# Optimization experiments

Measured on AMD Instinct MI355X. Metric: run time of the kernel, lower is better.

## Reference

```python
import jax, jax.numpy as jnp
import numpy as np

N = 50000      # nodes
E = 800000     # edges (avg degree 16)
D_IN = 128     # input_dim
H = 64         # hidden_dim (== output_dim)
L = 3          # num_layers


def setup_inputs() -> dict:
    key = jax.random.key(0)
    ks = jax.random.split(key, 24)
    s = 0.05
    p = lambda k, shape: jax.random.normal(k, shape, dtype=jnp.float32) * s
    inp = {}
    inp["node_features"] = jax.random.normal(ks[0], (N, D_IN), dtype=jnp.float32)
    inp["edge_index"] = jax.random.randint(ks[1], (2, E), 0, N, dtype=jnp.int32)
    # pre_mlp: Linear-ReLU-Linear (setup_LRL_nn with hidden_sizes=[hidden_dim])
    inp["pre_w1"] = p(ks[2], (D_IN, H)); inp["pre_b1"] = jnp.zeros((H,), jnp.float32)
    inp["pre_w2"] = p(ks[3], (H, H));    inp["pre_b2"] = jnp.zeros((H,), jnp.float32)
    # learnable skip gates (initialized to ones as in the module)
    inp["skip"] = jnp.ones((L, L), jnp.float32)
    # SAGEConv layers: lin_l (on mean-aggregated neighbors, with bias) + lin_r (root)
    for i in range(L):
        din = H * (i + 1)
        inp[f"wl{i}"] = p(ks[4 + 3 * i], (din, H))
        inp[f"bl{i}"] = jnp.zeros((H,), jnp.float32)
        inp[f"wr{i}"] = p(ks[5 + 3 * i], (din, H))
    # post_mlp: 256->64, 64->64, 64->256, 256->64
    inp["post_w1"] = p(ks[14], (H * (L + 1), H)); inp["post_b1"] = jnp.zeros((H,), jnp.float32)
    inp["post_w2"] = p(ks[15], (H, H));           inp["post_b2"] = jnp.zeros((H,), jnp.float32)
    inp["post_w3"] = p(ks[16], (H, 256));         inp["post_b3"] = jnp.zeros((256,), jnp.float32)
    inp["post_w4"] = p(ks[17], (256, H));         inp["post_b4"] = jnp.zeros((H,), jnp.float32)
    return inp


def _sage(x, src, dst, inv_deg, wl, bl, wr):
    # PyG SAGEConv (mean aggr): lin_l(mean_{j->i} x_j) + lin_r(x_i)
    agg = jax.ops.segment_sum(x[src], dst, num_segments=N) * inv_deg  # [N, Din]
    return agg @ wl + bl + x @ wr


def reference(node_features, edge_index,
              pre_w1, pre_b1, pre_w2, pre_b2, skip,
              wl0, bl0, wr0, wl1, bl1, wr1, wl2, bl2, wr2,
              post_w1, post_b1, post_w2, post_b2, post_w3, post_b3, post_w4, post_b4):
    src, dst = edge_index[0], edge_index[1]
    deg = jax.ops.segment_sum(jnp.ones((E,), jnp.float32), dst, num_segments=N)
    inv_deg = (1.0 / jnp.maximum(deg, 1.0))[:, None]  # [N,1]

    # pre_mlp
    x = jax.nn.relu(node_features @ pre_w1 + pre_b1) @ pre_w2 + pre_b2  # [N,H]

    layers = [(wl0, bl0, wr0), (wl1, bl1, wr1), (wl2, bl2, wr2)]
    all_emb = [x]
    emb = x
    for i, (wl, bl, wr) in enumerate(layers):
        gates = jax.nn.sigmoid(skip[i, :i + 1])  # [i+1]
        curr = jnp.concatenate([all_emb[j] * gates[j] for j in range(i + 1)], axis=1)  # [N, H*(i+1)]
        h = jax.nn.relu(_sage(curr, src, dst, inv_deg, wl, bl, wr))  # [N,H]  (dropout p=0)
        emb = jnp.concatenate([emb, h], axis=1)
        all_emb.append(h)

    s = jnp.sum(emb, axis=-2)  # sums over all nodes -> [H*(L+1)] (faithful to source)
    h = jax.nn.leaky_relu(s @ post_w1 + post_b1, negative_slope=0.1)
    h = jax.nn.relu(h @ post_w2 + post_b2)
    h = jax.nn.relu(h @ post_w3 + post_b3)
    return h @ post_w4 + post_b4  # [H]
```

## Files before the change

kernel.cpp:

```cpp
#include <hip/hip_runtime.h>
#include <math.h>

#define NN 50000
#define NE 800000
#define NB 196
#define SLOT 8192
#define PBH 8192

typedef float v4f __attribute__((ext_vector_type(4)));
typedef float v2f __attribute__((ext_vector_type(2)));
typedef _Float16 v8h __attribute__((ext_vector_type(8)));

__device__ __forceinline__ unsigned char enc8(float v) {
#if __has_builtin(__builtin_amdgcn_cvt_pk_fp8_f32)
  return (unsigned char)(__builtin_amdgcn_cvt_pk_fp8_f32(v, v, 0, false) & 0xFF);
#else
  unsigned u = __float_as_uint(v);
  unsigned s = (u >> 24) & 0x80u;
  unsigned au = u & 0x7fffffffu;
  float a = __uint_as_float(au);
  if (au < 0x3C800000u) {
    int m = (int)(a * 512.0f + 0.5f);
    if (m >= 8) return (unsigned char)(s | 8u);
    return (unsigned char)(s | (unsigned)m);
  }
  unsigned r = au + 0x7FFFFu + ((au >> 20) & 1u);
  unsigned e = (r >> 23) - 120u;
  unsigned man = (r >> 20) & 7u;
  if (e > 15u) { e = 15u; man = 6u; }
  return (unsigned char)(s | (e << 3) | man);
#endif
}

#if __has_builtin(__builtin_amdgcn_cvt_pk_f32_fp8)
#define DEC8_HW 1
#else
__device__ __forceinline__ float dec8_1(unsigned b) {
  unsigned s = (b & 0x80u) << 24;
  unsigned em = b & 0x7fu;
  float v;
  if (em >= 8u) v = __uint_as_float((((em >> 3) + 120u) << 23) | ((em & 7u) << 20));
  else v = (float)em * 0.001953125f;
  return __uint_as_float(__float_as_uint(v) | s);
}
#endif

__device__ __forceinline__ void dec8x8(uint2 u, float* f) {
#ifdef DEC8_HW
  v2f p0 = __builtin_amdgcn_cvt_pk_f32_fp8((int)u.x, false);
  v2f p1 = __builtin_amdgcn_cvt_pk_f32_fp8((int)u.x, true);
  v2f p2 = __builtin_amdgcn_cvt_pk_f32_fp8((int)u.y, false);
  v2f p3 = __builtin_amdgcn_cvt_pk_f32_fp8((int)u.y, true);
  f[0] = p0.x; f[1] = p0.y; f[2] = p1.x; f[3] = p1.y;
  f[4] = p2.x; f[5] = p2.y; f[6] = p3.x; f[7] = p3.y;
#else
#pragma unroll
  for (int i = 0; i < 4; ++i) f[i] = dec8_1((u.x >> (8 * i)) & 0xFF);
#pragma unroll
  for (int i = 0; i < 4; ++i) f[4 + i] = dec8_1((u.y >> (8 * i)) & 0xFF);
#endif
// ... 79 lines not shown
    if (e < NE) {
      int p = base[bk[i]] + lp[i];
      if (p < (bk[i] + 1) * SLOT) ebuf[p] = pk[i];
    }
  }
}

__global__ __launch_bounds__(256) void k_bbuild2(const unsigned* __restrict__ ebuf,
                                                 const int* __restrict__ gcur,
                                                 int* __restrict__ offs,
                                                 int* __restrict__ ends,
                                                 float* __restrict__ invd,
                                                 int* __restrict__ csr) {
  __shared__ int dcnt[256];
  __shared__ int cur[256];
  int t = threadIdx.x;
  int b = blockIdx.x;
  int node0 = b << 8;
  int es = b * SLOT;
  int ee = es + min(gcur[b], SLOT);
  dcnt[t] = 0;
  __syncthreads();
  for (int e = es + t; e < ee; e += 256) atomicAdd(&dcnt[ebuf[e] & 255], 1);
  __syncthreads();
  int v = dcnt[t];
  cur[t] = v;
  __syncthreads();
  for (int o = 1; o < 256; o <<= 1) {
    int u = (t >= o) ? cur[t - o] : 0;
    __syncthreads();
    cur[t] += u;
    __syncthreads();
  }
  int excl = cur[t] - v;
  int node = node0 + t;
  if (node < NN) {
    offs[node] = es + excl;
    ends[node] = es + excl + v;
    invd[node] = 1.0f / fmaxf((float)v, 1.0f);
  }
  __syncthreads();
  cur[t] = es + excl;
  __syncthreads();
  for (int e = es + t; e < ee; e += 256) {
    unsigned pk = ebuf[e];
    int p = atomicAdd(&cur[pk & 255], 1);
    csr[p] = (int)(pk >> 8);
  }
}

struct CArgs {
  const float* nf; const _Float16* wpk;
  const float* preb1; const float* preb2;
  const float* bl0; const float* bl1; const float* bl2;
  const int* offs; const int* ends; const int* csr; const float* invd;
  _Float16 *x, *h0, *h1, *m0, *m1;
  unsigned char *f8a, *f8b;
  float* sv;
  int* done;
  const float *pw1, *pb1, *pw2, *pb2, *pw3, *pb3, *pw4, *pb4;
  float* outp;
  int n;
};

__device__ __forceinline__ void gather_tile(int t, int n0,
    const unsigned char* __restrict__ fb, const int* __restrict__ offs,
    const int* __restrict__ ends, const int* __restrict__ csr,
    const float* __restrict__ invd,
    _Float16* atile, _Float16* mout, int n) {
  const int nd = t >> 2, q = t & 3;
  const int node = n0 + nd;
  float a[16];
#pragma unroll
  for (int i = 0; i < 16; ++i) a[i] = 0.f;
  float dinv = 0.f;
  if (node < n) {
    int s = offs[node], e = ends[node];
    dinv = invd[node];
    int p = s;
    for (; p + 4 <= e; p += 4) {
      int j0 = __builtin_nontemporal_load(csr + p);
      int j1 = __builtin_nontemporal_load(csr + p + 1);
      int j2 = __builtin_nontemporal_load(csr + p + 2);
      int j3 = __builtin_nontemporal_load(csr + p + 3);
      uint4 u0 = *(const uint4*)(fb + (size_t)j0 * 64 + q * 16);
      uint4 u1 = *(const uint4*)(fb + (size_t)j1 * 64 + q * 16);
      uint4 u2 = *(const uint4*)(fb + (size_t)j2 * 64 + q * 16);
      uint4 u3 = *(const uint4*)(fb + (size_t)j3 * 64 + q * 16);
      float f0[16], f1[16], f2[16], f3[16];
      dec8x16(u0, f0); dec8x16(u1, f1); dec8x16(u2, f2); dec8x16(u3, f3);
#pragma unroll
      for (int i = 0; i < 16; ++i) a[i] += (f0[i] + f1[i]) + (f2[i] + f3[i]);
    }
    for (; p < e; ++p) {
      int j = __builtin_nontemporal_load(csr + p);
      uint4 u = *(const uint4*)(fb + (size_t)j * 64 + q * 16);
      float f[16];
      dec8x16(u, f);
#pragma unroll
      for (int i = 0; i < 16; ++i) a[i] += f[i];
    }
  }
  v8h o0, o1;
#pragma unroll
  for (int i = 0; i < 8; ++i) {
    o0[i] = (_Float16)(a[i] * dinv);
    o1[i] = (_Float16)(a[8 + i] * dinv);
  }
  *(v8h*)(&atile[nd * 72 + q * 16]) = o0;
  *(v8h*)(&atile[nd * 72 + q * 16 + 8]) = o1;
  if (mout && node < n) {
    *(v8h*)(mout + (size_t)node * 64 + q * 16) = o0;
    *(v8h*)(mout + (size_t)node * 64 + q * 16 + 8) = o1;
  }
}

template <int NSRC, int FUSED>
__device__ __forceinline__ void lin_tile(int t, int tile, const CArgs& A,
    _Float16* atile,
    const _Float16* a0, const _Float16* a1, const _Float16* a2,
    const _Float16* a3, const _Float16* a4, const _Float16* a5,
    int pb0, int pb1, int pb2, int pb3, int pb4, int pb5,
    const unsigned char* gtab, const float* bias,
    _Float16* outp, unsigned char* out8, _Float16* mout, float* colsum) {
  const int lane = t & 63;
  const int wv   = t >> 6;
  const int qd   = lane >> 4;
  const int ln   = lane & 15;
  const int n0   = tile * 64;

  gather_tile(t, n0, gtab, A.offs, A.ends, A.csr, A.invd, atile, mout, A.n);
  __syncthreads();

  v4f acc[4];
#pragma unroll
  for (int ct = 0; ct < 4; ++ct) acc[ct] = (v4f){0.f, 0.f, 0.f, 0.f};

  const int arow = n0 + wv * 16 + ln;
  const bool arv = arow < A.n;
  const _Float16* srcs[6] = {a0, a1, a2, a3, a4, a5};
  const int pbs[6] = {pb0, pb1, pb2, pb3, pb4, pb5};

#pragma unroll
  for (int s = 0; s < NSRC; ++s) {
    v8h ah0, ah1;
    if (s == FUSED) {
      const _Float16* ph = atile + (wv * 16 + ln) * 72;
      ah0 = *(const v8h*)(ph + qd * 8);
      ah1 = *(const v8h*)(ph + 32 + qd * 8);
    } else if (arv) {
      const _Float16* ph = srcs[s] + (size_t)arow * 64;
      ah0 = *(const v8h*)(ph + qd * 8);
      ah1 = *(const v8h*)(ph + 32 + qd * 8);
    } else {
      v8h z;
#pragma unroll
      for (int j = 0; j < 8; ++j) z[j] = (_Float16)0.f;
      ah0 = ah1 = z;
    }
    const _Float16* pw = A.wpk + (size_t)pbs[s] * PBH;
#pragma unroll
    for (int ct = 0; ct < 4; ++ct) {
      const _Float16* pf0 = pw + (size_t)(ct * 64 + lane) * 8;
      const _Float16* pf1 = pw + (size_t)(512 + ct * 64 + lane) * 8;
      v8h bh0 = *(const v8h*)(pf0);
      v8h bl0v = *(const v8h*)(pf0 + 2048);
      v8h bh1 = *(const v8h*)(pf1);
      v8h bl1v = *(const v8h*)(pf1 + 2048);
      acc[ct] = __builtin_amdgcn_mfma_f32_16x16x32_f16(ah0, bh0, acc[ct], 0, 0, 0);
      acc[ct] = __builtin_amdgcn_mfma_f32_16x16x32_f16(ah0, bl0v, acc[ct], 0, 0, 0);
      acc[ct] = __builtin_amdgcn_mfma_f32_16x16x32_f16(ah1, bh1, acc[ct], 0, 0, 0);
      acc[ct] = __builtin_amdgcn_mfma_f32_16x16x32_f16(ah1, bl1v, acc[ct], 0, 0, 0);
    }
  }

  float bvals[4];
#pragma unroll
  for (int ct = 0; ct < 4; ++ct) bvals[ct] = bias[ct * 16 + ln];

  __syncthreads();
  unsigned char* f8t = (unsigned char*)atile;
  float* red = (float*)&atile[2304];

  float cs[4] = {0.f, 0.f, 0.f, 0.f};
#pragma unroll
  for (int ct = 0; ct < 4; ++ct) {
#pragma unroll
    for (int r = 0; r < 4; ++r) {
      int nb = wv * 16 + qd * 4 + r;
      int node = n0 + nb;
      float v = fmaxf(acc[ct][r] + bvals[ct], 0.f);
      if (node < A.n) {
        if (outp) outp[(size_t)node * 64 + ct * 16 + ln] = (_Float16)v;
        if (out8) f8t[nb * 64 + ct * 16 + ln] = enc8(v);
        cs[ct] += v;
      }
    }
  }
#pragma unroll
  for (int ct = 0; ct < 4; ++ct) {
    float v = cs[ct];
    v += __shfl_xor(v, 16, 64);
    v += __shfl_xor(v, 32, 64);
    if (qd == 0) red[wv * 64 + ct * 16 + ln] = v;
  }
  __syncthreads();
  if (out8) {
    int row = t >> 2, ch = t & 3;
    if (n0 + row < A.n) {
      uint4 val = *(const uint4*)(f8t + row * 64 + ch * 16);
      *(uint4*)(out8 + (size_t)(n0 + row) * 64 + ch * 16) = val;
    }
  }
  if (t < 64) {
    float ssum = red[t] + red[64 + t] + red[128 + t] + red[192 + t];
    atomicAdd(&colsum[t], ssum);
  }
}

__device__ __forceinline__ void pre_tile(int t, int tile, const CArgs& A,
                                         _Float16* atile) {
  const int lane = t & 63;
  const int wv   = t >> 6;
  const int qd   = lane >> 4;
  const int ln   = lane & 15;
  const int n0   = tile * 64;
  const int arow = n0 + wv * 16 + ln;
  const bool arv = arow < A.n;

  v4f acc[4];
#pragma unroll
  for (int ct = 0; ct < 4; ++ct) acc[ct] = (v4f){0.f, 0.f, 0.f, 0.f};
  v8h ah[2];

  auto domfma = [&](int pbi) {
    const _Float16* pw = A.wpk + (size_t)pbi * PBH;
#pragma unroll
    for (int ks = 0; ks < 2; ++ks) {
#pragma unroll
      for (int ct = 0; ct < 4; ++ct) {
        const _Float16* pf = pw + (size_t)(ks * 512 + ct * 64 + lane) * 8;
        v8h bh = *(const v8h*)(pf);
        v8h bl = *(const v8h*)(pf + 2048);
        acc[ct] = __builtin_amdgcn_mfma_f32_16x16x32_f16(ah[ks], bh, acc[ct], 0, 0, 0);
        acc[ct] = __builtin_amdgcn_mfma_f32_16x16x32_f16(ah[ks], bl, acc[ct], 0, 0, 0);
      }
    }
  };

  for (int s = 0; s < 2; ++s) {
#pragma unroll
    for (int ks = 0; ks < 2; ++ks) {
      v8h hv;
      if (arv) {
        const float* p = A.nf + (size_t)arow * 128 + s * 64 + ks * 32 + qd * 8;
        float4 u0 = *(const float4*)(p);
        float4 u1 = *(const float4*)(p + 4);
        hv[0] = (_Float16)u0.x; hv[1] = (_Float16)u0.y;
        hv[2] = (_Float16)u0.z; hv[3] = (_Float16)u0.w;
        hv[4] = (_Float16)u1.x; hv[5] = (_Float16)u1.y;
        hv[6] = (_Float16)u1.z; hv[7] = (_Float16)u1.w;
      } else {
#pragma unroll
        for (int j = 0; j < 8; ++j) hv[j] = (_Float16)0.f;
      }
      ah[ks] = hv;
    }
    domfma(s);
  }

  float b1v[4];
#pragma unroll
  for (int ct = 0; ct < 4; ++ct) b1v[ct] = A.preb1[ct * 16 + ln];
#pragma unroll
  for (int ct = 0; ct < 4; ++ct) {
#pragma unroll
    for (int r = 0; r < 4; ++r) {
      int nb = wv * 16 + qd * 4 + r;
      float v = fmaxf(acc[ct][r] + b1v[ct], 0.f);
// ... 1 lines not shown
    }
  }
#pragma unroll
  for (int ct = 0; ct < 4; ++ct) acc[ct] = (v4f){0.f, 0.f, 0.f, 0.f};
  __syncthreads();

  {
    const _Float16* ph = atile + (wv * 16 + ln) * 72;
    ah[0] = *(const v8h*)(ph + qd * 8);
    ah[1] = *(const v8h*)(ph + 32 + qd * 8);
  }
  domfma(2);

  float b2v[4];
#pragma unroll
  for (int ct = 0; ct < 4; ++ct) b2v[ct] = A.preb2[ct * 16 + ln];

  __syncthreads();
  unsigned char* f8t = (unsigned char*)atile;
  float* red = (float*)&atile[2304];
  float cs[4] = {0.f, 0.f, 0.f, 0.f};
#pragma unroll
  for (int ct = 0; ct < 4; ++ct) {
#pragma unroll
    for (int r = 0; r < 4; ++r) {
      int nb = wv * 16 + qd * 4 + r;
      int node = n0 + nb;
      float v = acc[ct][r] + b2v[ct];
      if (node < A.n) {
        A.x[(size_t)node * 64 + ct * 16 + ln] = (_Float16)v;
        f8t[nb * 64 + ct * 16 + ln] = enc8(v);
        cs[ct] += v;
      }
    }
  }
#pragma unroll
  for (int ct = 0; ct < 4; ++ct) {
    float v = cs[ct];
    v += __shfl_xor(v, 16, 64);
    v += __shfl_xor(v, 32, 64);
    if (qd == 0) red[wv * 64 + ct * 16 + ln] = v;
  }
  __syncthreads();
  {
    int row = t >> 2, ch = t & 3;
    if (n0 + row < A.n) {
      uint4 val = *(const uint4*)(f8t + row * 64 + ch * 16);
      *(uint4*)(A.f8a + (size_t)(n0 + row) * 64 + ch * 16) = val;
    }
  }
  if (t < 64) {
    float ssum = red[t] + red[64 + t] + red[128 + t] + red[192 + t];
    atomicAdd(&A.sv[t], ssum);
  }
}

__device__ __forceinline__ void post_body(int tt, const CArgs& A, float* Lf) {
  float* sh = Lf; float* h1 = Lf + 256; float* h2 = Lf + 320; float* h3 = Lf + 384;
  if (tt < 256) sh[tt] = atomicAdd(&A.sv[tt], 0.0f);
  __syncthreads();
  if (tt < 64) {
    float a = A.pb1[tt];
    for (int k = 0; k < 256; ++k) a += sh[k] * A.pw1[k * 64 + tt];
    h1[tt] = (a >= 0.f) ? a : 0.1f * a;
  }
  __syncthreads();
  if (tt < 64) {
    float a = A.pb2[tt];
    for (int k = 0; k < 64; ++k) a += h1[k] * A.pw2[k * 64 + tt];
    h2[tt] = fmaxf(a, 0.f);
  }
  __syncthreads();
  if (tt < 256) {
    float a = A.pb3[tt];
    for (int k = 0; k < 64; ++k) a += h2[k] * A.pw3[k * 256 + tt];
    h3[tt] = fmaxf(a, 0.f);
  }
  __syncthreads();
  if (tt < 64) {
    float a = A.pb4[tt];
    for (int k = 0; k < 256; ++k) a += h3[k] * A.pw4[k * 64 + tt];
    A.outp[tt] = a;
  }
}

__global__ __launch_bounds__(256) void k_preF(CArgs A) {
  __shared__ _Float16 atile[64 * 72];
  pre_tile(threadIdx.x, blockIdx.x, A, atile);
}

struct FLinArgs {
  CArgs C;
  const _Float16* a[6];
  int pb[6];
  const unsigned char* gtab;
  const float* bias;
  _Float16* outp;
  unsigned char* out8;
  _Float16* mout;
  float* colsum;
};

template <int NSRC, int FUSED, int DOPOST>
__global__ __launch_bounds__(256) void k_linF(FLinArgs F) {
  __shared__ _Float16 atile[64 * 72];
  __shared__ int lastflag;
  lin_tile<NSRC, FUSED>(threadIdx.x, blockIdx.x, F.C, atile,
                        F.a[0], F.a[1], F.a[2], F.a[3], F.a[4], F.a[5],
                        F.pb[0], F.pb[1], F.pb[2], F.pb[3], F.pb[4], F.pb[5],
                        F.gtab, F.bias, F.outp, F.out8, F.mout, F.colsum);
  if (DOPOST) {
    __syncthreads();
    __threadfence();
    if (threadIdx.x == 0)
      lastflag = (atomicAdd(F.C.done, 1) == (int)gridDim.x - 1);
    __syncthreads();
    if (lastflag) post_body(threadIdx.x, F.C, (float*)atile);
  }
}

extern "C" void kernel_launch(void* const* d_in, const int* in_sizes, int n_in,
                              void* d_out, int out_size, void* d_ws, size_t ws_size,
                              hipStream_t stream) {
  const float* nf     = (const float*)d_in[0];
  const int*   ei     = (const int*)d_in[1];
  const float* pre_w1 = (const float*)d_in[2];
  const float* pre_b1 = (const float*)d_in[3];
  const float* pre_w2 = (const float*)d_in[4];
  const float* pre_b2 = (const float*)d_in[5];
  const float* skip   = (const float*)d_in[6];
  const float* wl0 = (const float*)d_in[7],  *bl0 = (const float*)d_in[8],  *wr0 = (const float*)d_in[9];
  const float* wl1 = (const float*)d_in[10], *bl1 = (const float*)d_in[11], *wr1 = (const float*)d_in[12];
  const float* wl2 = (const float*)d_in[13], *bl2 = (const float*)d_in[14], *wr2 = (const float*)d_in[15];
  const float* pw1 = (const float*)d_in[16], *pb1 = (const float*)d_in[17];
  const float* pw2 = (const float*)d_in[18], *pb2 = (const float*)d_in[19];
  const float* pw3 = (const float*)d_in[20], *pb3 = (const float*)d_in[21];
  const float* pw4 = (const float*)d_in[22], *pb4 = (const float*)d_in[23];
  float* out = (float*)d_out;

  const int N = NN, E = NE;

  char* ws = (char*)d_ws;
  size_t pos = 0;
  auto alloc = [&](size_t bytes) {
    char* p = ws + pos;
    pos += (bytes + 255) & ~(size_t)255;
    return (void*)p;
  };
  int*      gcur  = (int*)alloc((size_t)NB * 4);
  unsigned* ebuf  = (unsigned*)alloc((size_t)NB * SLOT * 4);
  int*      offs  = (int*)alloc((size_t)N * 4);
  int*      ends  = (int*)alloc((size_t)N * 4);
  float*    invd  = (float*)alloc((size_t)N * 4);
  int*      csr   = (int*)alloc((size_t)NB * SLOT * 4);
  const size_t PB = (size_t)N * 64 * 2;
  _Float16* x  = (_Float16*)alloc(PB);
  _Float16* h0 = (_Float16*)alloc(PB);
  _Float16* h1 = (_Float16*)alloc(PB);
  _Float16* m0 = (_Float16*)alloc(PB);
  _Float16* m1 = (_Float16*)alloc(PB);
  unsigned char* f8a = (unsigned char*)alloc((size_t)N * 64);
  unsigned char* f8b = (unsigned char*)alloc((size_t)N * 64);
  _Float16* wpk = (_Float16*)alloc((size_t)15 * PBH * 2);
  float* sv = (float*)alloc(256 * 4);
  int* done = (int*)alloc(256);

  const int* e_src = ei;
  const int* e_dst = ei + E;
  const float* wsrc[15] = {pre_w1, pre_w1 + 64 * 64, pre_w2,
                           wl0, wr0,
                           wl1, wl1 + 64 * 64, wr1, wr1 + 64 * 64,
                           wl2, wl2 + 64 * 64, wl2 + 128 * 64,
                           wr2, wr2 + 64 * 64, wr2 + 128 * 64};
  const int gi[15] = {-1, -1, -1, 0, 0, 3, 4, 3, 4, 6, 7, 8, 6, 7, 8};

  {
    WPackArgs W;
    for (int i = 0; i < 15; ++i) { W.w[i] = wsrc[i]; W.gidx[i] = gi[i]; }
    W.skip = skip; W.outp = wpk;
    W.gcur = gcur; W.sv = sv; W.done = done;
    k_wpack<<<16, 256, 0, stream>>>(W);
  }

  const int EGRID = (E + 4095) / 4096;
  k_bscatter2<<<EGRID, 256, 0, stream>>>(e_src, e_dst, gcur, ebuf);
  k_bbuild2<<<NB, 256, 0, stream>>>(ebuf, gcur, offs, ends, invd, csr);

  CArgs C;
  C.nf = nf; C.wpk = wpk; C.preb1 = pre_b1; C.preb2 = pre_b2;
  C.bl0 = bl0; C.bl1 = bl1; C.bl2 = bl2;
  C.offs = offs; C.ends = ends; C.csr = csr; C.invd = invd;
  C.x = x; C.h0 = h0; C.h1 = h1; C.m0 = m0; C.m1 = m1;
  C.f8a = f8a; C.f8b = f8b; C.sv = sv; C.done = done;
  C.pw1 = pw1; C.pb1 = pb1; C.pw2 = pw2; C.pb2 = pb2;
  C.pw3 = pw3; C.pb3 = pb3; C.pw4 = pw4; C.pb4 = pb4;
  C.outp = out; C.n = N;

  const int LGRID = (N + 63) / 64;

  k_preF<<<LGRID, 256, 0, stream>>>(C);

  {
    FLinArgs F; F.C = C;
    F.a[0] = nullptr; F.a[1] = x; F.a[2] = nullptr; F.a[3] = nullptr;
    F.a[4] = nullptr; F.a[5] = nullptr;
    F.pb[0] = 3; F.pb[1] = 4; F.pb[2] = 0; F.pb[3] = 0; F.pb[4] = 0; F.pb[5] = 0;
    F.gtab = f8a; F.bias = bl0;
    F.outp = h0; F.out8 = f8b; F.mout = m0; F.colsum = sv + 64;
    k_linF<2, 0, 0><<<LGRID, 256, 0, stream>>>(F);
  }

  {
    FLinArgs F; F.C = C;
    F.a[0] = m0; F.a[1] = nullptr; F.a[2] = x; F.a[3] = h0;
    F.a[4] = nullptr; F.a[5] = nullptr;
    F.pb[0] = 5; F.pb[1] = 6; F.pb[2] = 7; F.pb[3] = 8; F.pb[4] = 0; F.pb[5] = 0;
    F.gtab = f8b; F.bias = bl1;
    F.outp = h1; F.out8 = f8a; F.mout = m1; F.colsum = sv + 128;
    k_linF<4, 1, 0><<<LGRID, 256, 0, stream>>>(F);
  }

  {
    FLinArgs F; F.C = C;
    F.a[0] = m0; F.a[1] = m1; F.a[2] = nullptr; F.a[3] = x;
    F.a[4] = h0; F.a[5] = h1;
    F.pb[0] = 9; F.pb[1] = 10; F.pb[2] = 11; F.pb[3] = 12; F.pb[4] = 13; F.pb[5] = 14;
    F.gtab = f8a; F.bias = bl2;
    F.outp = nullptr; F.out8 = nullptr; F.mout = nullptr; F.colsum = sv + 192;
    k_linF<6, 2, 1><<<LGRID, 256, 0, stream>>>(F);
  }
}
```

Measured before the change: 333.9 us.

## Double layer-kernel block to 512 threads, splitting gather edges and GEMM sources

The fused SAGE layer kernel now runs 512 threads per 64-node tile. During neighbor gathering, two threads share each node-quarter and process alternating edges; their partial sums are combined with a shuffle. The MFMA source loop is split between two wave groups, and one group's partial accumulators are reduced through a new shared-memory buffer. This adds more memory-level parallelism to the latency-bound gather, at the cost of extra shared memory, an extra barrier, and clamped redundant loads on short edge lists.

```diff
diff --git a/kernel.cpp b/kernel.cpp
--- a/kernel.cpp
+++ b/kernel.cpp
@@ -191,10 +191,9 @@
 struct CArgs {
   const float* nf; const _Float16* wpk;
   const float* preb1; const float* preb2;
-  const float* bl0; const float* bl1; const float* bl2;
   const int* offs; const int* ends; const int* csr; const float* invd;
-  _Float16 *x, *h0, *h1, *m0, *m1;
-  unsigned char *f8a, *f8b;
+  _Float16 *x;
+  unsigned char *f8a;
   float* sv;
   int* done;
   const float *pw1, *pb1, *pw2, *pb2, *pw3, *pb3, *pw4, *pb4;
@@ -202,168 +201,243 @@
   int n;
 };
 
-__device__ __forceinline__ void gather_tile(int t, int n0,
-    const unsigned char* __restrict__ fb, const int* __restrict__ offs,
-    const int* __restrict__ ends, const int* __restrict__ csr,
-    const float* __restrict__ invd,
-    _Float16* atile, _Float16* mout, int n) {
-  const int nd = t >> 2, q = t & 3;
-  const int node = n0 + nd;
-  float a[16];
-#pragma unroll
-  for (int i = 0; i < 16; ++i) a[i] = 0.f;
-  float dinv = 0.f;
-  if (node < n) {
-    int s = offs[node], e = ends[node];
-    dinv = invd[node];
-    int p = s;
-    for (; p + 4 <= e; p += 4) {
-      int j0 = __builtin_nontemporal_load(csr + p);
-      int j1 = __builtin_nontemporal_load(csr + p + 1);
-      int j2 = __builtin_nontemporal_load(csr + p + 2);
-      int j3 = __builtin_nontemporal_load(csr + p + 3);
-      uint4 u0 = *(const uint4*)(fb + (size_t)j0 * 64 + q * 16);
-      uint4 u1 = *(const uint4*)(fb + (size_t)j1 * 64 + q * 16);
-      uint4 u2 = *(const uint4*)(fb + (size_t)j2 * 64 + q * 16);
-      uint4 u3 = *(const uint4*)(fb + (size_t)j3 * 64 + q * 16);
-      float f0[16], f1[16], f2[16], f3[16];
-      dec8x16(u0, f0); dec8x16(u1, f1); dec8x16(u2, f2); dec8x16(u3, f3);
-#pragma unroll
-      for (int i = 0; i < 16; ++i) a[i] += (f0[i] + f1[i]) + (f2[i] + f3[i]);
-    }
-    for (; p < e; ++p) {
-      int j = __builtin_nontemporal_load(csr + p);
-      uint4 u = *(const uint4*)(fb + (size_t)j * 64 + q * 16);
-      float f[16];
-      dec8x16(u, f);
-#pragma unroll
-      for (int i = 0; i < 16; ++i) a[i] += f[i];
-    }
-  }
-  v8h o0, o1;
-#pragma unroll
-  for (int i = 0; i < 8; ++i) {
-    o0[i] = (_Float16)(a[i] * dinv);
-    o1[i] = (_Float16)(a[8 + i] * dinv);
-  }
-  *(v8h*)(&atile[nd * 72 + q * 16]) = o0;
-  *(v8h*)(&atile[nd * 72 + q * 16 + 8]) = o1;
-  if (mout && node < n) {
-    *(v8h*)(mout + (size_t)node * 64 + q * 16) = o0;
-    *(v8h*)(mout + (size_t)node * 64 + q * 16 + 8) = o1;
-  }
-}
-
-template <int NSRC, int FUSED>
-__device__ __forceinline__ void lin_tile(int t, int tile, const CArgs& A,
-    _Float16* atile,
-    const _Float16* a0, const _Float16* a1, const _Float16* a2,
-    const _Float16* a3, const _Float16* a4, const _Float16* a5,
-    int pb0, int pb1, int pb2, int pb3, int pb4, int pb5,
-    const unsigned char* gtab, const float* bias,
-    _Float16* outp, unsigned char* out8, _Float16* mout, float* colsum) {
+struct FLinArgs {
+  CArgs C;
+  const _Float16* a[6];
+  int pb[6];
+  const unsigned char* gtab;
+  const float* bias;
+  _Float16* outp;
+  unsigned char* out8;
+  _Float16* mout;
+  float* colsum;
+};
+
+__device__ __forceinline__ void post_body(int tt, const CArgs& A, float* Lf) {
+  float* sh = Lf; float* h1 = Lf + 256; float* h2 = Lf + 320; float* h3 = Lf + 384;
+  if (tt < 256) sh[tt] = atomicAdd(&A.sv[tt], 0.0f);
+  __syncthreads();
+  if (tt < 64) {
+    float a = A.pb1[tt];
+    for (int k = 0; k < 256; ++k) a += sh[k] * A.pw1[k * 64 + tt];
+    h1[tt] = (a >= 0.f) ? a : 0.1f * a;
+  }
+  __syncthreads();
+  if (tt < 64) {
+    float a = A.pb2[tt];
+    for (int k = 0; k < 64; ++k) a += h1[k] * A.pw2[k * 64 + tt];
+    h2[tt] = fmaxf(a, 0.f);
+  }
+  __syncthreads();
+  if (tt < 256) {
+    float a = A.pb3[tt];
+    for (int k = 0; k < 64; ++k) a += h2[k] * A.pw3[k * 256 + tt];
+    h3[tt] = fmaxf(a, 0.f);
+  }
+  __syncthreads();
+  if (tt < 64) {
+    float a = A.pb4[tt];
+    for (int k = 0; k < 256; ++k) a += h3[k] * A.pw4[k * 64 + tt];
+    A.outp[tt] = a;
+  }
+}
+
+template <int NSRC, int FUSED, int DOPOST>
+__global__ __launch_bounds__(512) void k_lin(FLinArgs F) {
+  __shared__ _Float16 atile[64 * 72];
+  __shared__ float cbuf[64 * 65];
+  __shared__ int lastflag;
+  const CArgs& C = F.C;
+  const int t    = threadIdx.x;
+  const int lane = t & 63;
+  const int w    = t >> 6;
+  const int wq   = w & 3;
+  const int sg   = w >> 2;
+  const int qd   = lane >> 4;
+  const int ln   = lane & 15;
+  const int n0   = blockIdx.x * 64;
+
+  {
+    const int nd = t >> 3;
+    const int sl = (t >> 2) & 1;
+    const int q  = t & 3;
+    const int node = n0 + nd;
+    float a[16];
+#pragma unroll
+    for (int i = 0; i < 16; ++i) a[i] = 0.f;
+    float dinv = 0.f;
+    if (node < C.n) {
+      int s = C.offs[node], e = C.ends[node];
+      dinv = C.invd[node];
+      const unsigned char* fb = F.gtab;
+      if (e > s) {
+        int emax = e - 1;
+        for (int p0 = s; p0 < e; p0 += 8) {
+          int pa = p0 + sl, pb_ = p0 + 2 + sl, pc = p0 + 4 + sl, pd = p0 + 6 + sl;
+          int ja = __builtin_nontemporal_load(C.csr + (pa < emax ? pa : emax));
+          int jb = __builtin_nontemporal_load(C.csr + (pb_ < emax ? pb_ : emax));
+          int jc = __builtin_nontemporal_load(C.csr + (pc < emax ? pc : emax));
+          int jd = __builtin_nontemporal_load(C.csr + (pd < emax ? pd : emax));
+          uint4 ua = *(const uint4*)(fb + (size_t)ja * 64 + q * 16);
+          uint4 ub = *(const uint4*)(fb + (size_t)jb * 64 + q * 16);
+          uint4 uc = *(const uint4*)(fb + (size_t)jc * 64 + q * 16);
+          uint4 ud = *(const uint4*)(fb + (size_t)jd * 64 + q * 16);
+          float f[16];
+          dec8x16(ua, f);
+          if (pa < e) {
+#pragma unroll
+            for (int i = 0; i < 16; ++i) a[i] += f[i];
+          }
+          dec8x16(ub, f);
+          if (pb_ < e) {
+#pragma unroll
+            for (int i = 0; i < 16; ++i) a[i] += f[i];
+          }
+          dec8x16(uc, f);
+          if (pc < e) {
+#pragma unroll
+            for (int i = 0; i < 16; ++i) a[i] += f[i];
+          }
+          dec8x16(ud, f);
+          if (pd < e) {
+#pragma unroll
+            for (int i = 0; i < 16; ++i) a[i] += f[i];
+          }
+        }
+      }
+    }
+#pragma unroll
+    for (int i = 0; i < 16; ++i) a[i] += __shfl_xor(a[i], 4, 64);
+    if (sl == 0) {
+      v8h o0, o1;
+#pragma unroll
+      for (int i = 0; i < 8; ++i) {
+        o0[i] = (_Float16)(a[i] * dinv);
+        o1[i] = (_Float16)(a[8 + i] * dinv);
+      }
+      *(v8h*)(&atile[nd * 72 + q * 16]) = o0;
+      *(v8h*)(&atile[nd * 72 + q * 16 + 8]) = o1;
+      if (F.mout && node < C.n) {
+        *(v8h*)(F.mout + (size_t)node * 64 + q * 16) = o0;
+        *(v8h*)(F.mout + (size_t)node * 64 + q * 16 + 8) = o1;
+      }
+    }
+  }
+  __syncthreads();
+
+  v4f acc[4];
+#pragma unroll
+  for (int ct = 0; ct < 4; ++ct) acc[ct] = (v4f){0.f, 0.f, 0.f, 0.f};
+
+  const int arow = n0 + wq * 16 + ln;
+  const bool arv = arow < C.n;
+  const int h = (NSRC + 1) >> 1;
+  const int sbeg = sg ? h : 0;
+  const int send = sg ? NSRC : h;
+  v8h ah[2];
+
+  for (int s = sbeg; s < send; ++s) {
+    if (s == FUSED) {
+      const _Float16* ph = atile + (wq * 16 + ln) * 72;
+      ah[0] = *(const v8h*)(ph + qd * 8);
+      ah[1] = *(const v8h*)(ph + 32 + qd * 8);
+    } else if (arv) {
+      const _Float16* ph = F.a[s] + (size_t)arow * 64;
+      ah[0] = *(const v8h*)(ph + qd * 8);
+      ah[1] = *(const v8h*)(ph + 32 + qd * 8);
+    } else {
+      v8h z;
+#pragma unroll
+      for (int j = 0; j < 8; ++j) z[j] = (_Float16)0.f;
+      ah[0] = ah[1] = z;
+    }
+    const _Float16* pw = C.wpk + (size_t)F.pb[s] * PBH;
+#pragma unroll
+    for (int ks = 0; ks < 2; ++ks) {
+#pragma unroll
+      for (int ct = 0; ct < 4; ++ct) {
+        const _Float16* pf = pw + (size_t)(ks * 512 + ct * 64 + lane) * 8;
+        v8h bh = *(const v8h*)(pf);
+        v8h bl = *(const v8h*)(pf + 2048);
+        acc[ct] = __builtin_amdgcn_mfma_f32_16x16x32_f16(ah[ks], bh, acc[ct], 0, 0, 0);
+        acc[ct] = __builtin_amdgcn_mfma_f32_16x16x32_f16(ah[ks], bl, acc[ct], 0, 0, 0);
+      }
+    }
+  }
+
+  if (sg == 1) {
+#pragma unroll
+    for (int ct = 0; ct < 4; ++ct)
+#pragma unroll
+      for (int r = 0; r < 4; ++r) {
+        int nb = wq * 16 + qd * 4 + r;
+        cbuf[nb * 65 + ct * 16 + ln] = acc[ct][r];
+      }
+  }
+  __syncthreads();
+
+  unsigned char* f8t = (unsigned char*)atile;
+  float* red = (float*)&atile[2304];
+
+  if (sg == 0) {
+    float bvals[4];
+#pragma unroll
+    for (int ct = 0; ct < 4; ++ct) bvals[ct] = F.bias[ct * 16 + ln];
+    float cs[4] = {0.f, 0.f, 0.f, 0.f};
+#pragma unroll
+    for (int ct = 0; ct < 4; ++ct) {
+#pragma unroll
+      for (int r = 0; r < 4; ++r) {
+        int nb = wq * 16 + qd * 4 + r;
+        int node = n0 + nb;
+        float v = acc[ct][r] + cbuf[nb * 65 + ct * 16 + ln] + bvals[ct];
+        v = fmaxf(v, 0.f);
+        if (node < C.n) {
+          if (F.outp) F.outp[(size_t)node * 64 + ct * 16 + ln] = (_Float16)v;
+          if (F.out8) f8t[nb * 64 + ct * 16 + ln] = enc8(v);
+          cs[ct] += v;
+        }
+      }
+    }
+#pragma unroll
+    for (int ct = 0; ct < 4; ++ct) {
+      float v = cs[ct];
+      v += __shfl_xor(v, 16, 64);
+      v += __shfl_xor(v, 32, 64);
+      if (qd == 0) red[wq * 64 + ct * 16 + ln] = v;
+    }
+  }
+  __syncthreads();
+  if (F.out8 && t < 256) {
+    int row = t >> 2, ch = t & 3;
+    if (n0 + row < C.n) {
+      uint4 val = *(const uint4*)(f8t + row * 64 + ch * 16);
+      *(uint4*)(F.out8 + (size_t)(n0 + row) * 64 + ch * 16) = val;
+    }
+  }
+  if (t < 64) {
+    float ssum = red[t] + red[64 + t] + red[128 + t] + red[192 + t];
+    atomicAdd(&F.colsum[t], ssum);
+  }
+
+  if (DOPOST) {
+    __syncthreads();
+    __threadfence();
+    if (t == 0)
+      lastflag = (atomicAdd(C.done, 1) == (int)gridDim.x - 1);
+    __syncthreads();
+    if (lastflag) post_body(t, C, (float*)atile);
+  }
+}
+
+__global__ __launch_bounds__(256) void k_preF(CArgs A) {
+  __shared__ _Float16 atile[64 * 72];
+  const int t    = threadIdx.x;
   const int lane = t & 63;
   const int wv   = t >> 6;
   const int qd   = lane >> 4;
   const int ln   = lane & 15;
-  const int n0   = tile * 64;
-
-  gather_tile(t, n0, gtab, A.offs, A.ends, A.csr, A.invd, atile, mout, A.n);
-  __syncthreads();
-
-  v4f acc[4];
-#pragma unroll
-  for (int ct = 0; ct < 4; ++ct) acc[ct] = (v4f){0.f, 0.f, 0.f, 0.f};
-
-  const int arow = n0 + wv * 16 + ln;
-  const bool arv = arow < A.n;
-  const _Float16* srcs[6] = {a0, a1, a2, a3, a4, a5};
-  const int pbs[6] = {pb0, pb1, pb2, pb3, pb4, pb5};
-
-#pragma unroll
-  for (int s = 0; s < NSRC; ++s) {
-    v8h ah0, ah1;
-    if (s == FUSED) {
-      const _Float16* ph = atile + (wv * 16 + ln) * 72;
-      ah0 = *(const v8h*)(ph + qd * 8);
-      ah1 = *(const v8h*)(ph + 32 + qd * 8);
-    } else if (arv) {
-      const _Float16* ph = srcs[s] + (size_t)arow * 64;
-      ah0 = *(const v8h*)(ph + qd * 8);
-      ah1 = *(const v8h*)(ph + 32 + qd * 8);
-    } else {
-      v8h z;
-#pragma unroll
-      for (int j = 0; j < 8; ++j) z[j] = (_Float16)0.f;
-      ah0 = ah1 = z;
-    }
-    const _Float16* pw = A.wpk + (size_t)pbs[s] * PBH;
-#pragma unroll
-    for (int ct = 0; ct < 4; ++ct) {
-      const _Float16* pf0 = pw + (size_t)(ct * 64 + lane) * 8;
-      const _Float16* pf1 = pw + (size_t)(512 + ct * 64 + lane) * 8;
-      v8h bh0 = *(const v8h*)(pf0);
-      v8h bl0v = *(const v8h*)(pf0 + 2048);
-      v8h bh1 = *(const v8h*)(pf1);
-      v8h bl1v = *(const v8h*)(pf1 + 2048);
-      acc[ct] = __builtin_amdgcn_mfma_f32_16x16x32_f16(ah0, bh0, acc[ct], 0, 0, 0);
-      acc[ct] = __builtin_amdgcn_mfma_f32_16x16x32_f16(ah0, bl0v, acc[ct], 0, 0, 0);
-      acc[ct] = __builtin_amdgcn_mfma_f32_16x16x32_f16(ah1, bh1, acc[ct], 0, 0, 0);
-      acc[ct] = __builtin_amdgcn_mfma_f32_16x16x32_f16(ah1, bl1v, acc[ct], 0, 0, 0);
-    }
-  }
-
-  float bvals[4];
-#pragma unroll
-  for (int ct = 0; ct < 4; ++ct) bvals[ct] = bias[ct * 16 + ln];
-
-  __syncthreads();
-  unsigned char* f8t = (unsigned char*)atile;
-  float* red = (float*)&atile[2304];
-
-  float cs[4] = {0.f, 0.f, 0.f, 0.f};
-#pragma unroll
-  for (int ct = 0; ct < 4; ++ct) {
-#pragma unroll
-    for (int r = 0; r < 4; ++r) {
-      int nb = wv * 16 + qd * 4 + r;
-      int node = n0 + nb;
-      float v = fmaxf(acc[ct][r] + bvals[ct], 0.f);
-      if (node < A.n) {
-        if (outp) outp[(size_t)node * 64 + ct * 16 + ln] = (_Float16)v;
-        if (out8) f8t[nb * 64 + ct * 16 + ln] = enc8(v);
-        cs[ct] += v;
-      }
-    }
-  }
-#pragma unroll
-  for (int ct = 0; ct < 4; ++ct) {
-    float v = cs[ct];
-    v += __shfl_xor(v, 16, 64);
-    v += __shfl_xor(v, 32, 64);
-    if (qd == 0) red[wv * 64 + ct * 16 + ln] = v;
-  }
-  __syncthreads();
-  if (out8) {
-    int row = t >> 2, ch = t & 3;
-    if (n0 + row < A.n) {
-      uint4 val = *(const uint4*)(f8t + row * 64 + ch * 16);
-      *(uint4*)(out8 + (size_t)(n0 + row) * 64 + ch * 16) = val;
-    }
-  }
-  if (t < 64) {
-    float ssum = red[t] + red[64 + t] + red[128 + t] + red[192 + t];
-    atomicAdd(&colsum[t], ssum);
-  }
-}
-
-__device__ __forceinline__ void pre_tile(int t, int tile, const CArgs& A,
-                                         _Float16* atile) {
-  const int lane = t & 63;
-  const int wv   = t >> 6;
-  const int qd   = lane >> 4;
-  const int ln   = lane & 15;
-  const int n0   = tile * 64;
+  const int n0   = blockIdx.x * 64;
   const int arow = n0 + wv * 16 + ln;
   const bool arv = arow < A.n;
 
@@ -471,70 +545,6 @@
   if (t < 64) {
     float ssum = red[t] + red[64 + t] + red[128 + t] + red[192 + t];
     atomicAdd(&A.sv[t], ssum);
-  }
-}
-
-__device__ __forceinline__ void post_body(int tt, const CArgs& A, float* Lf) {
-  float* sh = Lf; float* h1 = Lf + 256; float* h2 = Lf + 320; float* h3 = Lf + 384;
-  if (tt < 256) sh[tt] = atomicAdd(&A.sv[tt], 0.0f);
-  __syncthreads();
-  if (tt < 64) {
-    float a = A.pb1[tt];
-    for (int k = 0; k < 256; ++k) a += sh[k] * A.pw1[k * 64 + tt];
-    h1[tt] = (a >= 0.f) ? a : 0.1f * a;
-  }
-  __syncthreads();
-  if (tt < 64) {
-    float a = A.pb2[tt];
-    for (int k = 0; k < 64; ++k) a += h1[k] * A.pw2[k * 64 + tt];
-    h2[tt] = fmaxf(a, 0.f);
-  }
-  __syncthreads();
-  if (tt < 256) {
-    float a = A.pb3[tt];
-    for (int k = 0; k < 64; ++k) a += h2[k] * A.pw3[k * 256 + tt];
-    h3[tt] = fmaxf(a, 0.f);
-  }
-  __syncthreads();
-  if (tt < 64) {
-    float a = A.pb4[tt];
-    for (int k = 0; k < 256; ++k) a += h3[k] * A.pw4[k * 64 + tt];
-    A.outp[tt] = a;
-  }
-}
-
-__global__ __launch_bounds__(256) void k_preF(CArgs A) {
-  __shared__ _Float16 atile[64 * 72];
-  pre_tile(threadIdx.x, blockIdx.x, A, atile);
-}
-
-struct FLinArgs {
-  CArgs C;
-  const _Float16* a[6];
-  int pb[6];
-  const unsigned char* gtab;
-  const float* bias;
-  _Float16* outp;
-  unsigned char* out8;
-  _Float16* mout;
-  float* colsum;
-};
-
-template <int NSRC, int FUSED, int DOPOST>
-__global__ __launch_bounds__(256) void k_linF(FLinArgs F) {
-  __shared__ _Float16 atile[64 * 72];
-  __shared__ int lastflag;
-  lin_tile<NSRC, FUSED>(threadIdx.x, blockIdx.x, F.C, atile,
-                        F.a[0], F.a[1], F.a[2], F.a[3], F.a[4], F.a[5],
-                        F.pb[0], F.pb[1], F.pb[2], F.pb[3], F.pb[4], F.pb[5],
-                        F.gtab, F.bias, F.outp, F.out8, F.mout, F.colsum);
-  if (DOPOST) {
-    __syncthreads();
-    __threadfence();
-    if (threadIdx.x == 0)
-      lastflag = (atomicAdd(F.C.done, 1) == (int)gridDim.x - 1);
-    __syncthreads();
-    if (lastflag) post_body(threadIdx.x, F.C, (float*)atile);
   }
 }
 
@@ -607,10 +617,8 @@
 
   CArgs C;
   C.nf = nf; C.wpk = wpk; C.preb1 = pre_b1; C.preb2 = pre_b2;
-  C.bl0 = bl0; C.bl1 = bl1; C.bl2 = bl2;
   C.offs = offs; C.ends = ends; C.csr = csr; C.invd = invd;
-  C.x = x; C.h0 = h0; C.h1 = h1; C.m0 = m0; C.m1 = m1;
-  C.f8a = f8a; C.f8b = f8b; C.sv = sv; C.done = done;
+  C.x = x; C.f8a = f8a; C.sv = sv; C.done = done;
   C.pw1 = pw1; C.pb1 = pb1; C.pw2 = pw2; C.pb2 = pb2;
   C.pw3 = pw3; C.pb3 = pb3; C.pw4 = pw4; C.pb4 = pb4;
   C.outp = out; C.n = N;
@@ -626,7 +634,7 @@
     F.pb[0] = 3; F.pb[1] = 4; F.pb[2] = 0; F.pb[3] = 0; F.pb[4] = 0; F.pb[5] = 0;
     F.gtab = f8a; F.bias = bl0;
     F.outp = h0; F.out8 = f8b; F.mout = m0; F.colsum = sv + 64;
-    k_linF<2, 0, 0><<<LGRID, 256, 0, stream>>>(F);
+    k_lin<2, 0, 0><<<LGRID, 512, 0, stream>>>(F);
   }
 
   {
@@ -636,7 +644,7 @@
     F.pb[0] = 5; F.pb[1] = 6; F.pb[2] = 7; F.pb[3] = 8; F.pb[4] = 0; F.pb[5] = 0;
     F.gtab = f8b; F.bias = bl1;
     F.outp = h1; F.out8 = f8a; F.mout = m1; F.colsum = sv + 128;
-    k_linF<4, 1, 0><<<LGRID, 256, 0, stream>>>(F);
+    k_lin<4, 1, 0><<<LGRID, 512, 0, stream>>>(F);
   }
 
   {
@@ -646,6 +654,6 @@
     F.pb[0] = 9; F.pb[1] = 10; F.pb[2] = 11; F.pb[3] = 12; F.pb[4] = 13; F.pb[5] = 14;
     F.gtab = f8a; F.bias = bl2;
     F.outp = nullptr; F.out8 = nullptr; F.mout = nullptr; F.colsum = sv + 192;
-    k_linF<6, 2, 1><<<LGRID, 256, 0, stream>>>(F);
-  }
-}
+    k_lin<6, 2, 1><<<LGRID, 512, 0, stream>>>(F);
+  }
+}
```

Measured after the change: 390.6 us. 1.17x slower.

## Stage neighbor rows into LDS via async global_load_lds before accumulation

Applied to the files above, without the earlier changes.

The neighbor gather in each linear layer kernel now processes the tile's CSR edge range in chunks of 768. It loads the indices into shared memory, then uses global_load_lds to bring every neighbor's fp8 row into LDS in parallel across all waves. Each thread then accumulates its node's rows from LDS. This replaces per-thread dependent index-then-row global loads, increasing memory-level parallelism. The cost is about 50KB of LDS per block, which lowers occupancy, plus extra barriers per chunk.

```diff
diff --git a/kernel.cpp b/kernel.cpp
--- a/kernel.cpp
+++ b/kernel.cpp
@@ -6,6 +6,7 @@
 #define NB 196
 #define SLOT 8192
 #define PBH 8192
+#define CH  768
 
 typedef float v4f __attribute__((ext_vector_type(4)));
 typedef float v2f __attribute__((ext_vector_type(2)));
@@ -191,10 +192,9 @@
 struct CArgs {
   const float* nf; const _Float16* wpk;
   const float* preb1; const float* preb2;
-  const float* bl0; const float* bl1; const float* bl2;
   const int* offs; const int* ends; const int* csr; const float* invd;
-  _Float16 *x, *h0, *h1, *m0, *m1;
-  unsigned char *f8a, *f8b;
+  _Float16 *x;
+  unsigned char *f8a;
   float* sv;
   int* done;
   const float *pw1, *pb1, *pw2, *pb2, *pw3, *pb3, *pw4, *pb4;
@@ -202,73 +202,116 @@
   int n;
 };
 
-__device__ __forceinline__ void gather_tile(int t, int n0,
-    const unsigned char* __restrict__ fb, const int* __restrict__ offs,
-    const int* __restrict__ ends, const int* __restrict__ csr,
-    const float* __restrict__ invd,
-    _Float16* atile, _Float16* mout, int n) {
-  const int nd = t >> 2, q = t & 3;
-  const int node = n0 + nd;
-  float a[16];
-#pragma unroll
-  for (int i = 0; i < 16; ++i) a[i] = 0.f;
-  float dinv = 0.f;
-  if (node < n) {
-    int s = offs[node], e = ends[node];
-    dinv = invd[node];
-    int p = s;
-    for (; p + 4 <= e; p += 4) {
-      int j0 = __builtin_nontemporal_load(csr + p);
-      int j1 = __builtin_nontemporal_load(csr + p + 1);
-      int j2 = __builtin_nontemporal_load(csr + p + 2);
-      int j3 = __builtin_nontemporal_load(csr + p + 3);
-      uint4 u0 = *(const uint4*)(fb + (size_t)j0 * 64 + q * 16);
-      uint4 u1 = *(const uint4*)(fb + (size_t)j1 * 64 + q * 16);
-      uint4 u2 = *(const uint4*)(fb + (size_t)j2 * 64 + q * 16);
-      uint4 u3 = *(const uint4*)(fb + (size_t)j3 * 64 + q * 16);
-      float f0[16], f1[16], f2[16], f3[16];
-      dec8x16(u0, f0); dec8x16(u1, f1); dec8x16(u2, f2); dec8x16(u3, f3);
-#pragma unroll
-      for (int i = 0; i < 16; ++i) a[i] += (f0[i] + f1[i]) + (f2[i] + f3[i]);
-    }
-    for (; p < e; ++p) {
-      int j = __builtin_nontemporal_load(csr + p);
-      uint4 u = *(const uint4*)(fb + (size_t)j * 64 + q * 16);
-      float f[16];
-      dec8x16(u, f);
-#pragma unroll
-      for (int i = 0; i < 16; ++i) a[i] += f[i];
-    }
-  }
-  v8h o0, o1;
-#pragma unroll
-  for (int i = 0; i < 8; ++i) {
-    o0[i] = (_Float16)(a[i] * dinv);
-    o1[i] = (_Float16)(a[8 + i] * dinv);
-  }
-  *(v8h*)(&atile[nd * 72 + q * 16]) = o0;
-  *(v8h*)(&atile[nd * 72 + q * 16 + 8]) = o1;
-  if (mout && node < n) {
-    *(v8h*)(mout + (size_t)node * 64 + q * 16) = o0;
-    *(v8h*)(mout + (size_t)node * 64 + q * 16 + 8) = o1;
-  }
-}
-
-template <int NSRC, int FUSED>
-__device__ __forceinline__ void lin_tile(int t, int tile, const CArgs& A,
-    _Float16* atile,
-    const _Float16* a0, const _Float16* a1, const _Float16* a2,
-    const _Float16* a3, const _Float16* a4, const _Float16* a5,
-    int pb0, int pb1, int pb2, int pb3, int pb4, int pb5,
-    const unsigned char* gtab, const float* bias,
-    _Float16* outp, unsigned char* out8, _Float16* mout, float* colsum) {
+struct FLinArgs {
+  CArgs C;
+  const _Float16* a[6];
+  int pb[6];
+  const unsigned char* gtab;
+  const float* bias;
+  _Float16* outp;
+  unsigned char* out8;
+  _Float16* mout;
+  float* colsum;
+};
+
+__device__ __forceinline__ void post_body(int tt, const CArgs& A, float* Lf) {
+  float* sh = Lf; float* h1 = Lf + 256; float* h2 = Lf + 320; float* h3 = Lf + 384;
+  if (tt < 256) sh[tt] = atomicAdd(&A.sv[tt], 0.0f);
+  __syncthreads();
+  if (tt < 64) {
+    float a = A.pb1[tt];
+    for (int k = 0; k < 256; ++k) a += sh[k] * A.pw1[k * 64 + tt];
+    h1[tt] = (a >= 0.f) ? a : 0.1f * a;
+  }
+  __syncthreads();
+  if (tt < 64) {
+    float a = A.pb2[tt];
+    for (int k = 0; k < 64; ++k) a += h1[k] * A.pw2[k * 64 + tt];
+    h2[tt] = fmaxf(a, 0.f);
+  }
+  __syncthreads();
+  if (tt < 256) {
+    float a = A.pb3[tt];
+    for (int k = 0; k < 64; ++k) a += h2[k] * A.pw3[k * 256 + tt];
+    h3[tt] = fmaxf(a, 0.f);
+  }
+  __syncthreads();
+  if (tt < 64) {
+    float a = A.pb4[tt];
+    for (int k = 0; k < 256; ++k) a += h3[k] * A.pw4[k * 64 + tt];
+    A.outp[tt] = a;
+  }
+}
+
+template <int NSRC, int FUSED, int DOPOST>
+__global__ __launch_bounds__(256) void k_lin(FLinArgs F) {
+  __shared__ unsigned char rows[CH * 64];
+  __shared__ int sidx[CH];
+  __shared__ _Float16 atile[64 * 72];
+  __shared__ int lastflag;
+  const CArgs& C = F.C;
+  const int t    = threadIdx.x;
   const int lane = t & 63;
   const int wv   = t >> 6;
   const int qd   = lane >> 4;
   const int ln   = lane & 15;
-  const int n0   = tile * 64;
-
-  gather_tile(t, n0, gtab, A.offs, A.ends, A.csr, A.invd, atile, mout, A.n);
+  const int n0   = blockIdx.x * 64;
+
+  {
+    const int nd = t >> 2, q = t & 3;
+    const int node = n0 + nd;
+    const int lastn = min(n0 + 63, C.n - 1);
+    const int base = C.offs[n0];
+    const int ecnt = C.ends[lastn] - base;
+    float a[16];
+#pragma unroll
+    for (int i = 0; i < 16; ++i) a[i] = 0.f;
+    int ms = 0, me = 0;
+    float dinv = 0.f;
+    if (node < C.n) {
+      ms = C.offs[node] - base;
+      me = C.ends[node] - base;
+      dinv = C.invd[node];
+    }
+    for (int c0 = 0; c0 < ecnt; c0 += CH) {
+      int cn = min(CH, ecnt - c0);
+      for (int i = t; i < cn; i += 256) sidx[i] = C.csr[base + c0 + i];
+      __syncthreads();
+      int nch = (cn + 15) >> 4;
+      for (int k = wv; k < nch; k += 4) {
+        int r = k * 16 + (lane >> 2);
+        int idx = sidx[r < cn ? r : cn - 1];
+        const unsigned char* g = F.gtab + (size_t)idx * 64 + (size_t)(lane & 3) * 16;
+        __builtin_amdgcn_global_load_lds(
+            (const __attribute__((address_space(1))) unsigned int*)g,
+            (__attribute__((address_space(3))) unsigned int*)(rows + k * 1024),
+            16, 0, 0);
+      }
+      __syncthreads();
+      int ps = ms - c0; if (ps < 0) ps = 0;
+      int pe = me - c0; if (pe > cn) pe = cn;
+      for (int p = ps; p < pe; ++p) {
+        uint4 u = *(const uint4*)(rows + p * 64 + q * 16);
+        float f[16];
+        dec8x16(u, f);
+#pragma unroll
+        for (int i = 0; i < 16; ++i) a[i] += f[i];
+      }
+      __syncthreads();
+    }
+    v8h o0, o1;
+#pragma unroll
+    for (int i = 0; i < 8; ++i) {
+      o0[i] = (_Float16)(a[i] * dinv);
+      o1[i] = (_Float16)(a[8 + i] * dinv);
+    }
+    *(v8h*)(&atile[nd * 72 + q * 16]) = o0;
+    *(v8h*)(&atile[nd * 72 + q * 16 + 8]) = o1;
+    if (F.mout && node < C.n) {
+      *(v8h*)(F.mout + (size_t)node * 64 + q * 16) = o0;
+      *(v8h*)(F.mout + (size_t)node * 64 + q * 16 + 8) = o1;
+    }
+  }
   __syncthreads();
 
   v4f acc[4];
@@ -276,9 +319,7 @@
   for (int ct = 0; ct < 4; ++ct) acc[ct] = (v4f){0.f, 0.f, 0.f, 0.f};
 
   const int arow = n0 + wv * 16 + ln;
-  const bool arv = arow < A.n;
-  const _Float16* srcs[6] = {a0, a1, a2, a3, a4, a5};
-  const int pbs[6] = {pb0, pb1, pb2, pb3, pb4, pb5};
+  const bool arv = arow < C.n;
 
 #pragma unroll
   for (int s = 0; s < NSRC; ++s) {
@@ -288,7 +329,7 @@
       ah0 = *(const v8h*)(ph + qd * 8);
       ah1 = *(const v8h*)(ph + 32 + qd * 8);
     } else if (arv) {
-      const _Float16* ph = srcs[s] + (size_t)arow * 64;
+      const _Float16* ph = F.a[s] + (size_t)arow * 64;
       ah0 = *(const v8h*)(ph + qd * 8);
       ah1 = *(const v8h*)(ph + 32 + qd * 8);
     } else {
@@ -297,7 +338,7 @@
       for (int j = 0; j < 8; ++j) z[j] = (_Float16)0.f;
       ah0 = ah1 = z;
     }
-    const _Float16* pw = A.wpk + (size_t)pbs[s] * PBH;
+    const _Float16* pw = C.wpk + (size_t)F.pb[s] * PBH;
 #pragma unroll
     for (int ct = 0; ct < 4; ++ct) {
       const _Float16* pf0 = pw + (size_t)(ct * 64 + lane) * 8;
@@ -315,7 +356,7 @@
 
   float bvals[4];
 #pragma unroll
-  for (int ct = 0; ct < 4; ++ct) bvals[ct] = bias[ct * 16 + ln];
+  for (int ct = 0; ct < 4; ++ct) bvals[ct] = F.bias[ct * 16 + ln];
 
   __syncthreads();
   unsigned char* f8t = (unsigned char*)atile;
@@ -329,9 +370,9 @@
       int nb = wv * 16 + qd * 4 + r;
       int node = n0 + nb;
       float v = fmaxf(acc[ct][r] + bvals[ct], 0.f);
-      if (node < A.n) {
-        if (outp) outp[(size_t)node * 64 + ct * 16 + ln] = (_Float16)v;
-        if (out8) f8t[nb * 64 + ct * 16 + ln] = enc8(v);
+      if (node < C.n) {
+        if (F.outp) F.outp[(size_t)node * 64 + ct * 16 + ln] = (_Float16)v;
+        if (F.out8) f8t[nb * 64 + ct * 16 + ln] = enc8(v);
         cs[ct] += v;
       }
     }
@@ -344,26 +385,36 @@
     if (qd == 0) red[wv * 64 + ct * 16 + ln] = v;
   }
   __syncthreads();
-  if (out8) {
+  if (F.out8) {
     int row = t >> 2, ch = t & 3;
-    if (n0 + row < A.n) {
+    if (n0 + row < C.n) {
       uint4 val = *(const uint4*)(f8t + row * 64 + ch * 16);
-      *(uint4*)(out8 + (size_t)(n0 + row) * 64 + ch * 16) = val;
+      *(uint4*)(F.out8 + (size_t)(n0 + row) * 64 + ch * 16) = val;
     }
   }
   if (t < 64) {
     float ssum = red[t] + red[64 + t] + red[128 + t] + red[192 + t];
-    atomicAdd(&colsum[t], ssum);
-  }
-}
-
-__device__ __forceinline__ void pre_tile(int t, int tile, const CArgs& A,
-                                         _Float16* atile) {
+    atomicAdd(&F.colsum[t], ssum);
+  }
+
+  if (DOPOST) {
+    __syncthreads();
+    __threadfence();
+    if (t == 0)
+      lastflag = (atomicAdd(C.done, 1) == (int)gridDim.x - 1);
+    __syncthreads();
+    if (lastflag) post_body(t, C, (float*)atile);
+  }
+}
+
+__global__ __launch_bounds__(256) void k_preF(CArgs A) {
+  __shared__ _Float16 atile[64 * 72];
+  const int t    = threadIdx.x;
   const int lane = t & 63;
   const int wv   = t >> 6;
   const int qd   = lane >> 4;
   const int ln   = lane & 15;
-  const int n0   = tile * 64;
+  const int n0   = blockIdx.x * 64;
   const int arow = n0 + wv * 16 + ln;
   const bool arv = arow < A.n;
 
@@ -471,70 +522,6 @@
   if (t < 64) {
     float ssum = red[t] + red[64 + t] + red[128 + t] + red[192 + t];
     atomicAdd(&A.sv[t], ssum);
-  }
-}
-
-__device__ __forceinline__ void post_body(int tt, const CArgs& A, float* Lf) {
-  float* sh = Lf; float* h1 = Lf + 256; float* h2 = Lf + 320; float* h3 = Lf + 384;
-  if (tt < 256) sh[tt] = atomicAdd(&A.sv[tt], 0.0f);
-  __syncthreads();
-  if (tt < 64) {
-    float a = A.pb1[tt];
-    for (int k = 0; k < 256; ++k) a += sh[k] * A.pw1[k * 64 + tt];
-    h1[tt] = (a >= 0.f) ? a : 0.1f * a;
-  }
-  __syncthreads();
-  if (tt < 64) {
-    float a = A.pb2[tt];
-    for (int k = 0; k < 64; ++k) a += h1[k] * A.pw2[k * 64 + tt];
-    h2[tt] = fmaxf(a, 0.f);
-  }
-  __syncthreads();
-  if (tt < 256) {
-    float a = A.pb3[tt];
-    for (int k = 0; k < 64; ++k) a += h2[k] * A.pw3[k * 256 + tt];
-    h3[tt] = fmaxf(a, 0.f);
-  }
-  __syncthreads();
-  if (tt < 64) {
-    float a = A.pb4[tt];
-    for (int k = 0; k < 256; ++k) a += h3[k] * A.pw4[k * 64 + tt];
-    A.outp[tt] = a;
-  }
-}
-
-__global__ __launch_bounds__(256) void k_preF(CArgs A) {
-  __shared__ _Float16 atile[64 * 72];
-  pre_tile(threadIdx.x, blockIdx.x, A, atile);
-}
-
-struct FLinArgs {
-  CArgs C;
-  const _Float16* a[6];
-  int pb[6];
-  const unsigned char* gtab;
-  const float* bias;
-  _Float16* outp;
-  unsigned char* out8;
-  _Float16* mout;
-  float* colsum;
-};
-
-template <int NSRC, int FUSED, int DOPOST>
-__global__ __launch_bounds__(256) void k_linF(FLinArgs F) {
-  __shared__ _Float16 atile[64 * 72];
-  __shared__ int lastflag;
-  lin_tile<NSRC, FUSED>(threadIdx.x, blockIdx.x, F.C, atile,
-                        F.a[0], F.a[1], F.a[2], F.a[3], F.a[4], F.a[5],
-                        F.pb[0], F.pb[1], F.pb[2], F.pb[3], F.pb[4], F.pb[5],
-                        F.gtab, F.bias, F.outp, F.out8, F.mout, F.colsum);
-  if (DOPOST) {
-    __syncthreads();
-    __threadfence();
-    if (threadIdx.x == 0)
-      lastflag = (atomicAdd(F.C.done, 1) == (int)gridDim.x - 1);
-    __syncthreads();
-    if (lastflag) post_body(threadIdx.x, F.C, (float*)atile);
   }
 }
 
@@ -607,10 +594,8 @@
 
   CArgs C;
   C.nf = nf; C.wpk = wpk; C.preb1 = pre_b1; C.preb2 = pre_b2;
-  C.bl0 = bl0; C.bl1 = bl1; C.bl2 = bl2;
   C.offs = offs; C.ends = ends; C.csr = csr; C.invd = invd;
-  C.x = x; C.h0 = h0; C.h1 = h1; C.m0 = m0; C.m1 = m1;
-  C.f8a = f8a; C.f8b = f8b; C.sv = sv; C.done = done;
+  C.x = x; C.f8a = f8a; C.sv = sv; C.done = done;
   C.pw1 = pw1; C.pb1 = pb1; C.pw2 = pw2; C.pb2 = pb2;
   C.pw3 = pw3; C.pb3 = pb3; C.pw4 = pw4; C.pb4 = pb4;
   C.outp = out; C.n = N;
@@ -626,7 +611,7 @@
     F.pb[0] = 3; F.pb[1] = 4; F.pb[2] = 0; F.pb[3] = 0; F.pb[4] = 0; F.pb[5] = 0;
     F.gtab = f8a; F.bias = bl0;
     F.outp = h0; F.out8 = f8b; F.mout = m0; F.colsum = sv + 64;
-    k_linF<2, 0, 0><<<LGRID, 256, 0, stream>>>(F);
+    k_lin<2, 0, 0><<<LGRID, 256, 0, stream>>>(F);
   }
 
   {
@@ -636,7 +621,7 @@
     F.pb[0] = 5; F.pb[1] = 6; F.pb[2] = 7; F.pb[3] = 8; F.pb[4] = 0; F.pb[5] = 0;
     F.gtab = f8b; F.bias = bl1;
     F.outp = h1; F.out8 = f8a; F.mout = m1; F.colsum = sv + 128;
-    k_linF<4, 1, 0><<<LGRID, 256, 0, stream>>>(F);
+    k_lin<4, 1, 0><<<LGRID, 256, 0, stream>>>(F);
   }
 
   {
@@ -646,6 +631,6 @@
     F.pb[0] = 9; F.pb[1] = 10; F.pb[2] = 11; F.pb[3] = 12; F.pb[4] = 13; F.pb[5] = 14;
     F.gtab = f8a; F.bias = bl2;
     F.outp = nullptr; F.out8 = nullptr; F.mout = nullptr; F.colsum = sv + 192;
-    k_linF<6, 2, 1><<<LGRID, 256, 0, stream>>>(F);
-  }
-}
+    k_lin<6, 2, 1><<<LGRID, 256, 0, stream>>>(F);
+  }
+}
```

After: 350.6 us. +5.0%, slower.
